# Performance work log

Hardware: AMD Instinct MI355X
Metric: run time of the kernel (lower is better)

Reference implementation:

```python
import jax, jax.numpy as jnp
import numpy as np

D = 1024
H = 16
DK = D // H


def setup_inputs() -> dict:
    key = jax.random.key(0)
    ks = jax.random.split(key, 5)
    B, S = 4, 2048
    scale = 1.0 / np.sqrt(D)
    return {
        "inputs": jax.random.normal(ks[0], (B, S, D), dtype=jnp.float32),
        "mask": jnp.ones((B, S), dtype=jnp.int32),
        "Wq": jax.random.normal(ks[1], (D, D), dtype=jnp.float32) * scale,
        "Wk": jax.random.normal(ks[2], (D, D), dtype=jnp.float32) * scale,
        "Wv": jax.random.normal(ks[3], (D, D), dtype=jnp.float32) * scale,
        "Wo": jax.random.normal(ks[4], (D, D), dtype=jnp.float32) * scale,
    }


def reference(inputs, mask, Wq, Wk, Wv, Wo):
    B, S, _ = inputs.shape

    def split_heads(x):  # [B,S,D] -> [B,H,S,DK]
        return x.reshape(B, S, H, DK).transpose(0, 2, 1, 3)

    q = split_heads(inputs @ Wq)
    k = split_heads(inputs @ Wk)
    v = split_heads(inputs @ Wv)

    scores = jnp.einsum("bhqd,bhkd->bhqk", q, k) / jnp.sqrt(jnp.float32(DK))
    m = mask.astype(jnp.float32)[:, None, None, :]  # [B,1,1,S] over key axis
    scores = scores + (1.0 - m) * -1e9
    attn = jax.nn.softmax(scores, axis=-1)
    out = jnp.einsum("bhqk,bhkd->bhqd", attn, v)
    out = out.transpose(0, 2, 1, 3).reshape(B, S, D)
    return out @ Wo
```

## Files before the change

kernel.cpp:

```cpp
#include <hip/hip_runtime.h>
#include <hip/hip_bf16.h>
#include <stdint.h>

#define S_LEN 2048
#define D_DIM 1024
#define NH    16
#define DKH   64
#define BATCH 4

typedef __bf16 bf16x8 __attribute__((ext_vector_type(8)));
typedef float  f32x4  __attribute__((ext_vector_type(4)));

__device__ __forceinline__ unsigned short f2bf(float x) {
  unsigned u = __float_as_uint(x);
  return (unsigned short)((u + 0x7FFFu + ((u >> 16) & 1u)) >> 16);
}
__device__ __forceinline__ float bf2f(unsigned short b) {
  return __uint_as_float(((unsigned)b) << 16);
}

__device__ __forceinline__ void gll16(const void* g, void* l) {
  __builtin_amdgcn_global_load_lds((const __attribute__((address_space(1))) unsigned*)g,
                                   (__attribute__((address_space(3))) unsigned*)l, 16, 0, 0);
}

#define MFMA(a, b, c) __builtin_amdgcn_mfma_f32_16x16x32_bf16(a, b, c, 0, 0, 0)

__global__ void k_split(const float4* __restrict__ x, ushort4* __restrict__ hi,
                        ushort4* __restrict__ lo, int n4) {
  int i = blockIdx.x * 256 + threadIdx.x;
  if (i >= n4) return;
  float4 v = x[i];
  ushort4 h, l;
  h.x = f2bf(v.x); l.x = f2bf(v.x - bf2f(h.x));
  h.y = f2bf(v.y); l.y = f2bf(v.y - bf2f(h.y));
  h.z = f2bf(v.z); l.z = f2bf(v.z - bf2f(h.z));
  h.w = f2bf(v.w); l.w = f2bf(v.w - bf2f(h.w));
  hi[i] = h;
  lo[i] = l;
}

__global__ void k_wt(const float* __restrict__ W, unsigned short* __restrict__ hi,
                     unsigned short* __restrict__ lo) {
  __shared__ float t[64][65];
  const int tid = threadIdx.x;
  const int k0 = blockIdx.x * 64, n0 = blockIdx.y * 64;
#pragma unroll
  for (int i = 0; i < 16; i++) {
    int idx = i * 256 + tid;
    int r = idx >> 6, c = idx & 63;
    t[r][c] = W[(size_t)(k0 + r) * D_DIM + n0 + c];
  }
  __syncthreads();
#pragma unroll
  for (int i = 0; i < 16; i++) {
    int idx = i * 256 + tid;
    int r = idx >> 6, c = idx & 63;
    float v = t[c][r];
    unsigned short h = f2bf(v);
    size_t o = (size_t)(n0 + r) * D_DIM + k0 + c;
    hi[o] = h;
    lo[o] = f2bf(v - bf2f(h));
  }
}

__device__ __forceinline__ void gemm_core(
    const unsigned short* __restrict__ Ahi, const unsigned short* __restrict__ Alo,
    const unsigned short* __restrict__ Bth, const unsigned short* __restrict__ Btl,
    int m0, int n0, char* smem, f32x4 (&acc)[4][4]) {
  constexpr int K = 1024;
  char* sAh = smem;
  char* sAl = smem + 16384;
  char* sBh = smem + 32768;
  char* sBl = smem + 49152;

  const int tid = threadIdx.x;
  const int lane = tid & 63, w = tid >> 6;
  const int wr = w >> 1, wc = w & 1;

  int gofs[4], lofs[4];
#pragma unroll
  for (int i = 0; i < 4; i++) {
    int c = (w * 4 + i) * 64 + lane;
    int row = c >> 3, s = c & 7;
    int sp = s ^ (row & 7);
    gofs[i] = row * K + sp * 8;
    lofs[i] = (w * 4 + i) * 1024;
  }
  const unsigned short* pAh = Ahi + (size_t)m0 * K;
  const unsigned short* pAl = Alo + (size_t)m0 * K;
  const unsigned short* pBh = Bth + (size_t)n0 * K;
  const unsigned short* pBl = Btl + (size_t)n0 * K;

  for (int kt = 0; kt < K / 64; ++kt) {
    const int ko = kt * 64;
#pragma unroll
    for (int i = 0; i < 4; i++) {
      gll16(pAh + ko + gofs[i], sAh + lofs[i]);
      gll16(pAl + ko + gofs[i], sAl + lofs[i]);
      gll16(pBh + ko + gofs[i], sBh + lofs[i]);
      gll16(pBl + ko + gofs[i], sBl + lofs[i]);
    }
    __syncthreads();
#pragma unroll
    for (int kk = 0; kk < 2; kk++) {
      bf16x8 ah[4], al[4], bh[4], bl[4];
      const int cch = kk * 4 + (lane >> 4);
#pragma unroll
      for (int mr = 0; mr < 4; mr++) {
        int row = wr * 64 + mr * 16 + (lane & 15);
        int off = row * 128 + ((cch ^ (row & 7)) << 4);
        ah[mr] = *(const bf16x8*)(sAh + off);
        al[mr] = *(const bf16x8*)(sAl + off);
      }
#pragma unroll
      for (int nr = 0; nr < 4; nr++) {
        int row = wc * 64 + nr * 16 + (lane & 15);
        int off = row * 128 + ((cch ^ (row & 7)) << 4);
        bh[nr] = *(const bf16x8*)(sBh + off);
        bl[nr] = *(const bf16x8*)(sBl + off);
      }
#pragma unroll
      for (int mr = 0; mr < 4; mr++)
#pragma unroll
        for (int nr = 0; nr < 4; nr++) {
          acc[mr][nr] = MFMA(ah[mr], bh[nr], acc[mr][nr]);
          acc[mr][nr] = MFMA(ah[mr], bl[nr], acc[mr][nr]);
          acc[mr][nr] = MFMA(al[mr], bh[nr], acc[mr][nr]);
        }
    }
    __syncthreads();
  }
}

__global__ __launch_bounds__(256, 2) void gemm_qkv(
    const unsigned short* __restrict__ Ahi, const unsigned short* __restrict__ Alo,
    const unsigned short* __restrict__ Wqh, const unsigned short* __restrict__ Wql,
    const unsigned short* __restrict__ Wkh, const unsigned short* __restrict__ Wkl,
    const unsigned short* __restrict__ Wvh, const unsigned short* __restrict__ Wvl,
    unsigned short* __restrict__ Qh, unsigned short* __restrict__ Ql,
    unsigned short* __restrict__ Kh, unsigned short* __restrict__ Kl,
    unsigned short* __restrict__ Vth, unsigned short* __restrict__ Vtl) {
  constexpr int N = 1024;
  extern __shared__ char smem[];
  const int m0 = blockIdx.x * 128;
  const int mat = blockIdx.y >> 3;
  const int n0 = (blockIdx.y & 7) * 128;

  const unsigned short* Bth = mat == 0 ? Wqh : mat == 1 ? Wkh : Wvh;
  const unsigned short* Btl = mat == 0 ? Wql : mat == 1 ? Wkl : Wvl;
  unsigned short* Chi = mat == 0 ? Qh : mat == 1 ? Kh : Vth;
  unsigned short* Clo = mat == 0 ? Ql : mat == 1 ? Kl : Vtl;
  const float esc = mat == 1 ? 0.125f : 1.0f;

  f32x4 acc[4][4] = {};
  gemm_core(Ahi, Alo, Bth, Btl, m0, n0, smem, acc);

  const int lane = threadIdx.x & 63, w = threadIdx.x >> 6;
  const int wr = w >> 1, wc = w & 1;
#pragma unroll
  for (int mr = 0; mr < 4; mr++)
#pragma unroll
    for (int nr = 0; nr < 4; nr++)
#pragma unroll
      for (int j = 0; j < 4; j++) {
        int row = m0 + wr * 64 + mr * 16 + (lane >> 4) * 4 + j;
        int col = n0 + wc * 64 + nr * 16 + (lane & 15);
        float v = acc[mr][nr][j];
        if (mat < 2) {
          v *= esc;
          size_t o = (size_t)row * N + col;
          unsigned short hh = f2bf(v);
          Chi[o] = hh;
          Clo[o] = f2bf(v - bf2f(hh));
        } else {
          int bi = row >> 11, s = row & (S_LEN - 1);
          int hh2 = col >> 6, d = col & (DKH - 1);
          size_t o = ((size_t)(bi * NH + hh2) * DKH + d) * S_LEN + s;
          unsigned short hh = f2bf(v);
          Chi[o] = hh;
          Clo[o] = f2bf(v - bf2f(hh));
        }
      }
}

__global__ __launch_bounds__(256, 2) void gemm_wo(
    const unsigned short* __restrict__ Ahi, const unsigned short* __restrict__ Alo,
    const unsigned short* __restrict__ Bth, const unsigned short* __restrict__ Btl,
    float* __restrict__ Cf) {
  constexpr int N = 1024;
  extern __shared__ char smem[];
  const int m0 = blockIdx.x * 128, n0 = blockIdx.y * 128;

  f32x4 acc[4][4] = {};
  gemm_core(Ahi, Alo, Bth, Btl, m0, n0, smem, acc);

  const int lane = threadIdx.x & 63, w = threadIdx.x >> 6;
  const int wr = w >> 1, wc = w & 1;
#pragma unroll
  for (int mr = 0; mr < 4; mr++)
#pragma unroll
    for (int nr = 0; nr < 4; nr++)
#pragma unroll
      for (int j = 0; j < 4; j++) {
        int row = m0 + wr * 64 + mr * 16 + (lane >> 4) * 4 + j;
        int col = n0 + wc * 64 + nr * 16 + (lane & 15);
        Cf[(size_t)row * N + col] = acc[mr][nr][j];
      }
}

__global__ __launch_bounds__(256, 4) void attn5(
    const unsigned short* __restrict__ Qh, const unsigned short* __restrict__ Ql,
    const unsigned short* __restrict__ Kh, const unsigned short* __restrict__ Kl,
    const unsigned short* __restrict__ Vth, const unsigned short* __restrict__ Vtl,
    const int* __restrict__ mask,
    unsigned short* __restrict__ Oh, unsigned short* __restrict__ Ol) {
  __shared__ char sKh0[4096], sKl0[4096], sVh0[4096], sVl0[4096];
  __shared__ char sKh1[4096], sKl1[4096], sVh1[4096], sVl1[4096];
  __shared__ char sP[4][2048];

  const int tid = threadIdx.x, lane = tid & 63, w = tid >> 6;
  const int bh = blockIdx.x, b = bh >> 4, h = bh & (NH - 1);
  const int q0 = blockIdx.y * 128 + w * 32;
  const int lo16 = lane & 15, hi4 = lane >> 4;

  bf16x8 qh[2][2], ql[2][2];
#pragma unroll
  for (int g = 0; g < 2; g++)
#pragma unroll
    for (int kk = 0; kk < 2; kk++) {
      size_t base = ((size_t)(b * S_LEN + q0 + g * 16 + lo16)) * D_DIM + h * DKH + kk * 32 + hi4 * 8;
      qh[g][kk] = *(const bf16x8*)(Qh + base);
      ql[g][kk] = *(const bf16x8*)(Ql + base);
    }

  const int c = w * 64 + lane;
  const int krow = c >> 3;
  const int kcol = ((c & 7) ^ (krow & 7)) * 8;
  const int vrow = c >> 2;
  const int vcol = ((c & 3) ^ (vrow & 3)) * 8;
  const int ldst = w * 1024;

  float lsum[2][4] = {};
  f32x4 oacc[2][4] = {};
  char* sPw = sP[w];

  const size_t kbase = (size_t)b * S_LEN * D_DIM + h * DKH;
  const size_t vbase = (size_t)bh * DKH * S_LEN;
  const int* mrow = mask + b * S_LEN;

  auto STAGE = [&](char* dKh, char* dKl, char* dVh, char* dVl, int sk0) {
    size_t gk = kbase + (size_t)(sk0 + krow) * D_DIM + kcol;
    gll16(Kh + gk, dKh + ldst);
    gll16(Kl + gk, dKl + ldst);
    size_t gv = vbase + (size_t)vrow * S_LEN + sk0 + vcol;
    gll16(Vth + gv, dVh + ldst);
    gll16(Vtl + gv, dVl + ldst);
  };

  auto COMPUTE = [&](const char* cKh, const char* cKl, const char* cVh,
                     const char* cVl, int sk0) {
    f32x4 sc[2][2] = {};
    __builtin_amdgcn_s_setprio(1);
#pragma unroll
    for (int nr = 0; nr < 2; nr++) {
      int row = nr * 16 + lo16;
      int off0 = row * 128 + ((hi4 ^ (row & 7)) << 4);
      int off1 = row * 128 + (((4 + hi4) ^ (row & 7)) << 4);
      bf16x8 kh0 = *(const bf16x8*)(cKh + off0);
      bf16x8 kh1 = *(const bf16x8*)(cKh + off1);
      bf16x8 kl0 = *(const bf16x8*)(cKl + off0);
      bf16x8 kl1 = *(const bf16x8*)(cKl + off1);
#pragma unroll
      for (int g = 0; g < 2; g++) {
        sc[g][nr] = MFMA(qh[g][0], kh0, sc[g][nr]);
        sc[g][nr] = MFMA(qh[g][1], kh1, sc[g][nr]);
        sc[g][nr] = MFMA(qh[g][0], kl0, sc[g][nr]);
        sc[g][nr] = MFMA(qh[g][1], kl1, sc[g][nr]);
        sc[g][nr] = MFMA(ql[g][0], kh0, sc[g][nr]);
        sc[g][nr] = MFMA(ql[g][1], kh1, sc[g][nr]);
      }
    }
    __builtin_amdgcn_s_setprio(0);

#pragma unroll
    for (int nr = 0; nr < 2; nr++) {
      float bias = mrow[sk0 + nr * 16 + lo16] ? 0.f : -1e9f;
#pragma unroll
      for (int g = 0; g < 2; g++)
#pragma unroll
        for (int j = 0; j < 4; j++) {
          float p = __expf(sc[g][nr][j] + bias);
          lsum[g][j] += p;
          int row = g * 16 + hi4 * 4 + j;
          int colb = (nr * 16 + lo16) * 2;
          *(unsigned short*)(sPw + row * 64 + (colb ^ ((row & 3) << 4))) = f2bf(p);
        }
    }

    bf16x8 pa[2];
#pragma unroll
    for (int g = 0; g < 2; g++) {
      int row = g * 16 + lo16;
      pa[g] = *(const bf16x8*)(sPw + row * 64 + ((hi4 * 16) ^ ((row & 3) << 4)));
    }

    __builtin_amdgcn_s_setprio(1);
#pragma unroll
    for (int f = 0; f < 4; f++) {
      int vr = f * 16 + lo16;
      int voff = vr * 64 + ((hi4 ^ (vr & 3)) << 4);
      bf16x8 vh = *(const bf16x8*)(cVh + voff);
      bf16x8 vl = *(const bf16x8*)(cVl + voff);
#pragma unroll
      for (int g = 0; g < 2; g++) {
        oacc[g][f] = MFMA(pa[g], vh, oacc[g][f]);
        oacc[g][f] = MFMA(pa[g], vl, oacc[g][f]);
      }
    }
    __builtin_amdgcn_s_setprio(0);
  };

  STAGE(sKh0, sKl0, sVh0, sVl0, 0);
  __syncthreads();

  for (int kt = 0; kt < S_LEN / 32; kt += 2) {
    const int sk0 = kt * 32;
    STAGE(sKh1, sKl1, sVh1, sVl1, sk0 + 32);
    COMPUTE(sKh0, sKl0, sVh0, sVl0, sk0);
    __syncthreads();
    if (kt + 2 < S_LEN / 32) STAGE(sKh0, sKl0, sVh0, sVl0, sk0 + 64);
    COMPUTE(sKh1, sKl1, sVh1, sVl1, sk0 + 32);
    __syncthreads();
  }

  float inv[2][4];
#pragma unroll
  for (int g = 0; g < 2; g++)
#pragma unroll
    for (int j = 0; j < 4; j++) {
      float s = lsum[g][j];
      s += __shfl_xor(s, 1);
      s += __shfl_xor(s, 2);
      s += __shfl_xor(s, 4);
      s += __shfl_xor(s, 8);
      inv[g][j] = 1.f / s;
    }

#pragma unroll
  for (int g = 0; g < 2; g++)
#pragma unroll
    for (int f = 0; f < 4; f++)
#pragma unroll
      for (int j = 0; j < 4; j++) {
        int row = q0 + g * 16 + hi4 * 4 + j;
        int col = h * DKH + f * 16 + lo16;
        float v = oacc[g][f][j] * inv[g][j];
        size_t o = ((size_t)(b * S_LEN + row)) * D_DIM + col;
        unsigned short hh = f2bf(v);
        Oh[o] = hh;
        Ol[o] = f2bf(v - bf2f(hh));
      }
}

extern "C" void kernel_launch(void* const* d_in, const int* in_sizes, int n_in,
                              void* d_out, int out_size, void* d_ws, size_t ws_size,
                              hipStream_t stream) {
  const float* X = (const float*)d_in[0];
  const int* mask = (const int*)d_in[1];
  const float* Wq = (const float*)d_in[2];
  const float* Wk = (const float*)d_in[3];
  const float* Wv = (const float*)d_in[4];
  const float* Wo = (const float*)d_in[5];
  float* out = (float*)d_out;

  const size_t MB = 1024 * 1024;
  if (ws_size < 144 * MB) return;

  char* ws = (char*)d_ws;
  unsigned short* Xh = (unsigned short*)(ws);
  unsigned short* Xl = (unsigned short*)(ws + 16 * MB);
  unsigned short* Wqth = (unsigned short*)(ws + 32 * MB);
  unsigned short* Wqtl = Wqth + 1024 * 1024;
  unsigned short* Wkth = Wqtl + 1024 * 1024;
  unsigned short* Wktl = Wkth + 1024 * 1024;
  unsigned short* Wvth = Wktl + 1024 * 1024;
  unsigned short* Wvtl = Wvth + 1024 * 1024;
  unsigned short* Woth = Wvtl + 1024 * 1024;
  unsigned short* Wotl = Woth + 1024 * 1024;
  unsigned short* Qh = (unsigned short*)(ws + 48 * MB);
  unsigned short* Ql = (unsigned short*)(ws + 64 * MB);
  unsigned short* Kh = (unsigned short*)(ws + 80 * MB);
  unsigned short* Kl = (unsigned short*)(ws + 96 * MB);
  unsigned short* Vth = (unsigned short*)(ws + 112 * MB);
  unsigned short* Vtl = (unsigned short*)(ws + 128 * MB);

  const int n4 = BATCH * S_LEN * D_DIM / 4;
  k_split<<<(n4 + 255) / 256, 256, 0, stream>>>((const float4*)X, (ushort4*)Xh,
                                                (ushort4*)Xl, n4);
  dim3 wtg(16, 16);
  k_wt<<<wtg, 256, 0, stream>>>(Wq, Wqth, Wqtl);
  k_wt<<<wtg, 256, 0, stream>>>(Wk, Wkth, Wktl);
  k_wt<<<wtg, 256, 0, stream>>>(Wv, Wvth, Wvtl);
  k_wt<<<wtg, 256, 0, stream>>>(Wo, Woth, Wotl);

  gemm_qkv<<<dim3(64, 24), 256, 65536, stream>>>(
      Xh, Xl, Wqth, Wqtl, Wkth, Wktl, Wvth, Wvtl, Qh, Ql, Kh, Kl, Vth, Vtl);

  dim3 ag(BATCH * NH, S_LEN / 128);
  attn5<<<ag, 256, 0, stream>>>(Qh, Ql, Kh, Kl, Vth, Vtl, mask, Xh, Xl);

  gemm_wo<<<dim3(64, 8), 256, 65536, stream>>>(Xh, Xl, Woth, Wotl, out);
}
```

Measured before the change: 524.5 us.

## Widen attention key tile to 64, fuse weight transposes, use native bf16 convert

The attention kernel now stages 64 keys per tile instead of 32. Shared buffers and the P scratch double in size, the swizzles are widened to match, and the launch bound drops to 2 blocks per CU. This halves the number of barriers and staging rounds per block and gives more MFMA work per sync, but the larger LDS footprint lowers occupancy. Separately, the four weight-transpose launches are merged into one 3D-grid launch, and the float-to-bf16 rounding uses the compiler's native __bf16 conversion.

```diff
diff --git a/kernel.cpp b/kernel.cpp
--- a/kernel.cpp
+++ b/kernel.cpp
@@ -12,8 +12,7 @@
 typedef float  f32x4  __attribute__((ext_vector_type(4)));
 
 __device__ __forceinline__ unsigned short f2bf(float x) {
-  unsigned u = __float_as_uint(x);
-  return (unsigned short)((u + 0x7FFFu + ((u >> 16) & 1u)) >> 16);
+  return __builtin_bit_cast(unsigned short, (__bf16)x);
 }
 __device__ __forceinline__ float bf2f(unsigned short b) {
   return __uint_as_float(((unsigned)b) << 16);
@@ -40,9 +39,17 @@
   lo[i] = l;
 }
 
-__global__ void k_wt(const float* __restrict__ W, unsigned short* __restrict__ hi,
-                     unsigned short* __restrict__ lo) {
+__global__ void k_wt4(const float* __restrict__ W0, const float* __restrict__ W1,
+                      const float* __restrict__ W2, const float* __restrict__ W3,
+                      unsigned short* __restrict__ h0, unsigned short* __restrict__ l0,
+                      unsigned short* __restrict__ h1, unsigned short* __restrict__ l1,
+                      unsigned short* __restrict__ h2, unsigned short* __restrict__ l2,
+                      unsigned short* __restrict__ h3, unsigned short* __restrict__ l3) {
   __shared__ float t[64][65];
+  const int z = blockIdx.z;
+  const float* W = z == 0 ? W0 : z == 1 ? W1 : z == 2 ? W2 : W3;
+  unsigned short* hi = z == 0 ? h0 : z == 1 ? h1 : z == 2 ? h2 : h3;
+  unsigned short* lo = z == 0 ? l0 : z == 1 ? l1 : z == 2 ? l2 : l3;
   const int tid = threadIdx.x;
   const int k0 = blockIdx.x * 64, n0 = blockIdx.y * 64;
 #pragma unroll
@@ -209,15 +216,15 @@
       }
 }
 
-__global__ __launch_bounds__(256, 4) void attn5(
+__global__ __launch_bounds__(256, 2) void attn4(
     const unsigned short* __restrict__ Qh, const unsigned short* __restrict__ Ql,
     const unsigned short* __restrict__ Kh, const unsigned short* __restrict__ Kl,
     const unsigned short* __restrict__ Vth, const unsigned short* __restrict__ Vtl,
     const int* __restrict__ mask,
     unsigned short* __restrict__ Oh, unsigned short* __restrict__ Ol) {
-  __shared__ char sKh0[4096], sKl0[4096], sVh0[4096], sVl0[4096];
-  __shared__ char sKh1[4096], sKl1[4096], sVh1[4096], sVl1[4096];
-  __shared__ char sP[4][2048];
+  __shared__ char sKh0[8192], sKl0[8192], sVh0[8192], sVl0[8192];
+  __shared__ char sKh1[8192], sKl1[8192], sVh1[8192], sVl1[8192];
+  __shared__ char sP[4][4096];
 
   const int tid = threadIdx.x, lane = tid & 63, w = tid >> 6;
   const int bh = blockIdx.x, b = bh >> 4, h = bh & (NH - 1);
@@ -234,12 +241,15 @@
       ql[g][kk] = *(const bf16x8*)(Ql + base);
     }
 
-  const int c = w * 64 + lane;
-  const int krow = c >> 3;
-  const int kcol = ((c & 7) ^ (krow & 7)) * 8;
-  const int vrow = c >> 2;
-  const int vcol = ((c & 3) ^ (vrow & 3)) * 8;
-  const int ldst = w * 1024;
+  int srowK[2], scolK[2], lofs[2];
+#pragma unroll
+  for (int i = 0; i < 2; i++) {
+    int c = (w * 2 + i) * 64 + lane;
+    int row = c >> 3, s = c & 7;
+    srowK[i] = row;
+    scolK[i] = (s ^ (row & 7)) * 8;
+    lofs[i] = c * 16 - lane * 16;
+  }
 
   float lsum[2][4] = {};
   f32x4 oacc[2][4] = {};
@@ -250,20 +260,23 @@
   const int* mrow = mask + b * S_LEN;
 
   auto STAGE = [&](char* dKh, char* dKl, char* dVh, char* dVl, int sk0) {
-    size_t gk = kbase + (size_t)(sk0 + krow) * D_DIM + kcol;
-    gll16(Kh + gk, dKh + ldst);
-    gll16(Kl + gk, dKl + ldst);
-    size_t gv = vbase + (size_t)vrow * S_LEN + sk0 + vcol;
-    gll16(Vth + gv, dVh + ldst);
-    gll16(Vtl + gv, dVl + ldst);
+#pragma unroll
+    for (int i = 0; i < 2; i++) {
+      size_t gk = kbase + (size_t)(sk0 + srowK[i]) * D_DIM + scolK[i];
+      gll16(Kh + gk, dKh + lofs[i]);
+      gll16(Kl + gk, dKl + lofs[i]);
+      size_t gv = vbase + (size_t)srowK[i] * S_LEN + sk0 + scolK[i];
+      gll16(Vth + gv, dVh + lofs[i]);
+      gll16(Vtl + gv, dVl + lofs[i]);
+    }
   };
 
   auto COMPUTE = [&](const char* cKh, const char* cKl, const char* cVh,
                      const char* cVl, int sk0) {
-    f32x4 sc[2][2] = {};
+    f32x4 sc[2][4] = {};
     __builtin_amdgcn_s_setprio(1);
 #pragma unroll
-    for (int nr = 0; nr < 2; nr++) {
+    for (int nr = 0; nr < 4; nr++) {
       int row = nr * 16 + lo16;
       int off0 = row * 128 + ((hi4 ^ (row & 7)) << 4);
       int off1 = row * 128 + (((4 + hi4) ^ (row & 7)) << 4);
@@ -284,7 +297,7 @@
     __builtin_amdgcn_s_setprio(0);
 
 #pragma unroll
-    for (int nr = 0; nr < 2; nr++) {
+    for (int nr = 0; nr < 4; nr++) {
       float bias = mrow[sk0 + nr * 16 + lo16] ? 0.f : -1e9f;
 #pragma unroll
       for (int g = 0; g < 2; g++)
@@ -294,43 +307,48 @@
           lsum[g][j] += p;
           int row = g * 16 + hi4 * 4 + j;
           int colb = (nr * 16 + lo16) * 2;
-          *(unsigned short*)(sPw + row * 64 + (colb ^ ((row & 3) << 4))) = f2bf(p);
+          *(unsigned short*)(sPw + row * 128 + (colb ^ ((row & 7) << 4))) = f2bf(p);
         }
     }
 
-    bf16x8 pa[2];
-#pragma unroll
-    for (int g = 0; g < 2; g++) {
-      int row = g * 16 + lo16;
-      pa[g] = *(const bf16x8*)(sPw + row * 64 + ((hi4 * 16) ^ ((row & 3) << 4)));
-    }
+    bf16x8 pa[2][2];
+#pragma unroll
+    for (int g = 0; g < 2; g++)
+#pragma unroll
+      for (int kk = 0; kk < 2; kk++) {
+        int row = g * 16 + lo16;
+        int colb = kk * 64 + hi4 * 16;
+        pa[g][kk] = *(const bf16x8*)(sPw + row * 128 + (colb ^ ((row & 7) << 4)));
+      }
 
     __builtin_amdgcn_s_setprio(1);
 #pragma unroll
-    for (int f = 0; f < 4; f++) {
-      int vr = f * 16 + lo16;
-      int voff = vr * 64 + ((hi4 ^ (vr & 3)) << 4);
-      bf16x8 vh = *(const bf16x8*)(cVh + voff);
-      bf16x8 vl = *(const bf16x8*)(cVl + voff);
-#pragma unroll
-      for (int g = 0; g < 2; g++) {
-        oacc[g][f] = MFMA(pa[g], vh, oacc[g][f]);
-        oacc[g][f] = MFMA(pa[g], vl, oacc[g][f]);
-      }
-    }
+    for (int kk = 0; kk < 2; kk++)
+#pragma unroll
+      for (int f = 0; f < 4; f++) {
+        int vrow = f * 16 + lo16;
+        int voff = vrow * 128 + (((kk * 4 + hi4) ^ (vrow & 7)) << 4);
+        bf16x8 vh = *(const bf16x8*)(cVh + voff);
+        bf16x8 vl = *(const bf16x8*)(cVl + voff);
+#pragma unroll
+        for (int g = 0; g < 2; g++) {
+          oacc[g][f] = MFMA(pa[g][kk], vh, oacc[g][f]);
+          oacc[g][f] = MFMA(pa[g][kk], vl, oacc[g][f]);
+        }
+      }
     __builtin_amdgcn_s_setprio(0);
   };
 
   STAGE(sKh0, sKl0, sVh0, sVl0, 0);
   __syncthreads();
 
-  for (int kt = 0; kt < S_LEN / 32; kt += 2) {
-    const int sk0 = kt * 32;
-    STAGE(sKh1, sKl1, sVh1, sVl1, sk0 + 32);
+  for (int kt = 0; kt < S_LEN / 64; kt += 2) {
+    const int sk0 = kt * 64;
+    STAGE(sKh1, sKl1, sVh1, sVl1, sk0 + 64);
     COMPUTE(sKh0, sKl0, sVh0, sVl0, sk0);
     __syncthreads();
-    if (kt + 2 < S_LEN / 32) STAGE(sKh0, sKl0, sVh0, sVl0, sk0 + 64);
-    COMPUTE(sKh1, sKl1, sVh1, sVl1, sk0 + 32);
+    if (kt + 2 < S_LEN / 64) STAGE(sKh0, sKl0, sVh0, sVl0, sk0 + 128);
+    COMPUTE(sKh1, sKl1, sVh1, sVl1, sk0 + 64);
     __syncthreads();
   }
 
@@ -398,17 +416,15 @@
   const int n4 = BATCH * S_LEN * D_DIM / 4;
   k_split<<<(n4 + 255) / 256, 256, 0, stream>>>((const float4*)X, (ushort4*)Xh,
                                                 (ushort4*)Xl, n4);
-  dim3 wtg(16, 16);
-  k_wt<<<wtg, 256, 0, stream>>>(Wq, Wqth, Wqtl);
-  k_wt<<<wtg, 256, 0, stream>>>(Wk, Wkth, Wktl);
-  k_wt<<<wtg, 256, 0, stream>>>(Wv, Wvth, Wvtl);
-  k_wt<<<wtg, 256, 0, stream>>>(Wo, Woth, Wotl);
+  k_wt4<<<dim3(16, 16, 4), 256, 0, stream>>>(Wq, Wk, Wv, Wo,
+                                             Wqth, Wqtl, Wkth, Wktl,
+                                             Wvth, Wvtl, Woth, Wotl);
 
   gemm_qkv<<<dim3(64, 24), 256, 65536, stream>>>(
       Xh, Xl, Wqth, Wqtl, Wkth, Wktl, Wvth, Wvtl, Qh, Ql, Kh, Kl, Vth, Vtl);
 
   dim3 ag(BATCH * NH, S_LEN / 128);
-  attn5<<<ag, 256, 0, stream>>>(Qh, Ql, Kh, Kl, Vth, Vtl, mask, Xh, Xl);
+  attn4<<<ag, 256, 0, stream>>>(Qh, Ql, Kh, Kl, Vth, Vtl, mask, Xh, Xl);
 
   gemm_wo<<<dim3(64, 8), 256, 65536, stream>>>(Xh, Xl, Woth, Wotl, out);
 }
```

New measurement: 503.6 us. -4.0%, faster.
